# Kernel optimization log

Hardware: AMD Instinct MI355X
Metric: run time of the kernel (lower is better)

## Reference

```python
import jax, jax.numpy as jnp
import numpy as np

QUERY_DIM = 1024
KEY_DIM = 768
NUM_HEADS = 16
HEAD_DIM = QUERY_DIM // NUM_HEADS
SCALE = HEAD_DIM ** -0.5


def setup_inputs() -> dict:
    key = jax.random.key(0)
    ks = jax.random.split(key, 11)
    B, Nq, Nk = 4, 4096, 1024
    s_q = QUERY_DIM ** -0.5
    s_k = KEY_DIM ** -0.5
    return {
        "query": jax.random.normal(ks[0], (B, Nq, QUERY_DIM), jnp.float32),
        "key": jax.random.normal(ks[1], (B, Nk, KEY_DIM), jnp.float32),
        "value": jax.random.normal(ks[2], (B, Nk, KEY_DIM), jnp.float32),
        "Wq": jax.random.normal(ks[3], (QUERY_DIM, QUERY_DIM), jnp.float32) * s_q,
        "bq": jnp.zeros((QUERY_DIM,), jnp.float32),
        "Wk": jax.random.normal(ks[4], (KEY_DIM, QUERY_DIM), jnp.float32) * s_k,
        "bk": jnp.zeros((QUERY_DIM,), jnp.float32),
        "Wv": jax.random.normal(ks[5], (KEY_DIM, QUERY_DIM), jnp.float32) * s_k,
        "bv": jnp.zeros((QUERY_DIM,), jnp.float32),
        "Wo": jax.random.normal(ks[6], (QUERY_DIM, QUERY_DIM), jnp.float32) * s_q,
        "bo": jnp.zeros((QUERY_DIM,), jnp.float32),
    }


def reference(query, key, value, Wq, bq, Wk, bk, Wv, bv, Wo, bo):
    B, Nq, _ = query.shape
    Nk = key.shape[1]
    # projections to (B, H, N, d)
    q = (query @ Wq + bq).reshape(B, Nq, NUM_HEADS, HEAD_DIM).transpose(0, 2, 1, 3)
    k = (key @ Wk + bk).reshape(B, Nk, NUM_HEADS, HEAD_DIM).transpose(0, 2, 1, 3)
    v = (value @ Wv + bv).reshape(B, Nk, NUM_HEADS, HEAD_DIM).transpose(0, 2, 1, 3)
    attn = jnp.einsum("bhqd,bhkd->bhqk", q, k) * SCALE
    attn = jax.nn.softmax(attn, axis=-1)
    out = jnp.einsum("bhqk,bhkd->bhqd", attn, v)
    out = out.transpose(0, 2, 1, 3).reshape(B, Nq, QUERY_DIM)
    return out @ Wo + bo
```

## Files before the change

### kernel.cpp

```cpp
#include <hip/hip_runtime.h>
#include <hip/hip_bf16.h>
#include <stdint.h>


typedef unsigned short u16;
typedef __attribute__((ext_vector_type(8))) short short8;
typedef __attribute__((ext_vector_type(4))) float f32x4;

#define B_SZ 4
#define NQ   4096
#define NK   1024
#define QDIM 1024
#define KDIM 768
#define NH   16
#define HD   64
#define QSCALE (0.125f * 1.44269504f)

__device__ __forceinline__ u16 f2bf(float f) {
  union { float f; uint32_t u; } v; v.f = f;
  uint32_t u = v.u;
  return (u16)((u + 0x7FFFu + ((u >> 16) & 1u)) >> 16);
}

__device__ __forceinline__ uint32_t pk2(float a, float b) {
  union { __hip_bfloat162 h; uint32_t u; } cv;
  cv.h = __float22bfloat162_rn(float2{a, b});
  return cv.u;
}

__device__ __forceinline__ float fexp2(float x) {
  return __builtin_amdgcn_exp2f(x);
}

__device__ __forceinline__ void async16(u16* lds, const u16* g) {
  __builtin_amdgcn_global_load_lds(
      (__attribute__((address_space(1))) void*)(g),
      (__attribute__((address_space(3))) void*)(lds), 16, 0, 0);
}

__global__ __launch_bounds__(256) void f32_to_bf16_k(const float* __restrict__ in,
                                                     u16* __restrict__ out, int n4) {
  int i = blockIdx.x * 256 + threadIdx.x;
  if (i < n4) {
    f32x4 v = ((const f32x4*)in)[i];
    uint2 o = {pk2(v.x, v.y), pk2(v.z, v.w)};
    ((uint2*)out)[i] = o;
  }
}

__global__ __launch_bounds__(256) void f32_to_bf16_2k(const float* __restrict__ a,
                                                      const float* __restrict__ b,
                                                      u16* __restrict__ oa,
                                                      u16* __restrict__ ob, int n4) {
  int i = blockIdx.x * 256 + threadIdx.x;
  const float* in = blockIdx.y ? b : a;
  u16* out = blockIdx.y ? ob : oa;
  if (i < n4) {
    f32x4 v = ((const f32x4*)in)[i];
    uint2 o = {pk2(v.x, v.y), pk2(v.z, v.w)};
    ((uint2*)out)[i] = o;
  }
}

__global__ __launch_bounds__(256) void transpose_bf16_k(const float* __restrict__ W,
                                                        u16* __restrict__ Wt,
                                                        int K, int N) {
  __shared__ float t[32][33];
  int tx = threadIdx.x & 31, ty = threadIdx.x >> 5;
  int nb = blockIdx.x * 32, kb = blockIdx.y * 32;
#pragma unroll
  for (int i = 0; i < 4; ++i)
    t[ty + i * 8][tx] = W[(size_t)(kb + ty + i * 8) * N + nb + tx];
  __syncthreads();
#pragma unroll
  for (int i = 0; i < 4; ++i)
    Wt[(size_t)(nb + ty + i * 8) * K + kb + tx] = f2bf(t[tx][ty + i * 8]);
}

__global__ __launch_bounds__(256) void gemm_bt(const u16* __restrict__ A,
                                               const u16* __restrict__ Bt,
                                               const float* __restrict__ bias,
                                               float* __restrict__ Cf,
                                               u16* __restrict__ Cb,
                                               int M, int N, int K, int out_bf16,
                                               float scale) {
  __shared__ __align__(16) u16 Al[128 * 64];
  __shared__ __align__(16) u16 Bl[128 * 64];
  const int tid = threadIdx.x;
  const int w = tid >> 6, lane = tid & 63;
  const int g = lane >> 4, l15 = lane & 15;
  const int sw = l15 & 7;
  const int mbase = blockIdx.x * 128, nbase = blockIdx.y * 128;
  const int wm = (w & 1) * 64, wn = (w >> 1) * 64;

  f32x4 zero4 = {0.f, 0.f, 0.f, 0.f};
  f32x4 acc[4][4];
#pragma unroll
  for (int i = 0; i < 4; ++i)
#pragma unroll
    for (int j = 0; j < 4; ++j) acc[i][j] = zero4;

  for (int kb = 0; kb < K; kb += 64) {
#pragma unroll
    for (int i = 0; i < 4; ++i) {
      int cbase = w * 256 + i * 64;
      int c = cbase + lane;
      int row = c >> 3;
      int kc8 = ((c & 7) ^ (row & 7)) * 8;
      async16(&Al[cbase * 8], A + (size_t)(mbase + row) * K + kb + kc8);
      async16(&Bl[cbase * 8], Bt + (size_t)(nbase + row) * K + kb + kc8);
    }
    __syncthreads();
#pragma unroll
    for (int ks = 0; ks < 2; ++ks) {
      short8 af[4], bf[4];
#pragma unroll
      for (int mt = 0; mt < 4; ++mt)
        af[mt] = *(const short8*)&Al[(wm + mt * 16 + l15) * 64 + ((ks * 4 + g) ^ sw) * 8];
#pragma unroll
      for (int nt = 0; nt < 4; ++nt)
        bf[nt] = *(const short8*)&Bl[(wn + nt * 16 + l15) * 64 + ((ks * 4 + g) ^ sw) * 8];
#pragma unroll
      for (int mt = 0; mt < 4; ++mt)
#pragma unroll
        for (int nt = 0; nt < 4; ++nt)
          acc[mt][nt] = __builtin_amdgcn_mfma_f32_16x16x32_bf16(af[mt], bf[nt],
                                                                acc[mt][nt], 0, 0, 0);
    }
    __syncthreads();
  }

#pragma unroll
  for (int nt = 0; nt < 4; ++nt) {
    int col = nbase + wn + nt * 16 + l15;
    float bv = bias[col];
#pragma unroll
    for (int mt = 0; mt < 4; ++mt)
#pragma unroll
      for (int r = 0; r < 4; ++r) {
        int row = mbase + wm + mt * 16 + g * 4 + r;
        float v = (acc[mt][nt][r] + bv) * scale;
        if (out_bf16) Cb[(size_t)row * N + col] = f2bf(v);
        else          Cf[(size_t)row * N + col] = v;
      }
  }
}

__global__ __launch_bounds__(256) void gemm_kv(const u16* __restrict__ kA,
                                               const u16* __restrict__ vA,
                                               const u16* __restrict__ Wk,
                                               const u16* __restrict__ Wv,
                                               const float* __restrict__ bk,
                                               const float* __restrict__ bv,
                                               u16* __restrict__ Kp,
                                               u16* __restrict__ VT,
                                               int M, int N, int K) {
  __shared__ __align__(16) u16 Al[128 * 64];
  __shared__ __align__(16) u16 Bl[128 * 64];
  const int ct = blockIdx.z;
  const u16* A  = ct ? vA : kA;
  const u16* Bt = ct ? Wv : Wk;
  const float* bias = ct ? bv : bk;
  const int tid = threadIdx.x;
  const int w = tid >> 6, lane = tid & 63;
  const int g = lane >> 4, l15 = lane & 15;
  const int sw = l15 & 7;
  const int mbase = blockIdx.x * 128, nbase = blockIdx.y * 128;
  const int wm = (w & 1) * 64, wn = (w >> 1) * 64;

  f32x4 zero4 = {0.f, 0.f, 0.f, 0.f};
  f32x4 acc[4][4];
#pragma unroll
  for (int i = 0; i < 4; ++i)
#pragma unroll
    for (int j = 0; j < 4; ++j) acc[i][j] = zero4;

  for (int kb = 0; kb < K; kb += 64) {
#pragma unroll
    for (int i = 0; i < 4; ++i) {
      int cbase = w * 256 + i * 64;
      int c = cbase + lane;
      int row = c >> 3;
      int kc8 = ((c & 7) ^ (row & 7)) * 8;
      async16(&Al[cbase * 8], A + (size_t)(mbase + row) * K + kb + kc8);
      async16(&Bl[cbase * 8], Bt + (size_t)(nbase + row) * K + kb + kc8);
    }
    __syncthreads();
#pragma unroll
    for (int ks = 0; ks < 2; ++ks) {
      short8 af[4], bf[4];
#pragma unroll
      for (int mt = 0; mt < 4; ++mt)
        af[mt] = *(const short8*)&Al[(wm + mt * 16 + l15) * 64 + ((ks * 4 + g) ^ sw) * 8];
#pragma unroll
      for (int nt = 0; nt < 4; ++nt)
        bf[nt] = *(const short8*)&Bl[(wn + nt * 16 + l15) * 64 + ((ks * 4 + g) ^ sw) * 8];
      if (ct) {
#pragma unroll
        for (int nt = 0; nt < 4; ++nt)
#pragma unroll
          for (int mt = 0; mt < 4; ++mt)
            acc[nt][mt] = __builtin_amdgcn_mfma_f32_16x16x32_bf16(bf[nt], af[mt],
                                                                  acc[nt][mt], 0, 0, 0);
      } else {
#pragma unroll
        for (int mt = 0; mt < 4; ++mt)
#pragma unroll
          for (int nt = 0; nt < 4; ++nt)
            acc[mt][nt] = __builtin_amdgcn_mfma_f32_16x16x32_bf16(af[mt], bf[nt],
                                                                  acc[mt][nt], 0, 0, 0);
      }
    }
    __syncthreads();
  }

  if (ct) {
#pragma unroll
    for (int mt = 0; mt < 4; ++mt) {
      int m = mbase + wm + mt * 16 + l15;
#pragma unroll
      for (int nt = 0; nt < 4; ++nt)
#pragma unroll
        for (int r = 0; r < 4; ++r) {
          int n = nbase + wn + nt * 16 + g * 4 + r;
          VT[(size_t)n * M + m] = f2bf(acc[nt][mt][r] + bias[n]);
        }
    }
  } else {
#pragma unroll
    for (int nt = 0; nt < 4; ++nt) {
      int col = nbase + wn + nt * 16 + l15;
      float bvv = bias[col];
#pragma unroll
      for (int mt = 0; mt < 4; ++mt)
#pragma unroll
        for (int r = 0; r < 4; ++r) {
          int row = mbase + wm + mt * 16 + g * 4 + r;
          Kp[(size_t)row * N + col] = f2bf(acc[mt][nt][r] + bvv);
        }
    }
  }
}

__global__ __launch_bounds__(256) void attn_kernel(const u16* __restrict__ Qp,
                                                   const u16* __restrict__ Kp,
                                                   const u16* __restrict__ VT,
                                                   u16* __restrict__ AO) {
  __shared__ __align__(16) u16 K_lds[2][64 * 64];
  __shared__ __align__(16) u16 Vt_lds[2][64 * 64];
  __shared__ __align__(16) u16 P_lds[4][32 * 64];

  const int tid = threadIdx.x;
  const int w = tid >> 6, lane = tid & 63;
  const int g = lane >> 4, l15 = lane & 15;
  const int sw = l15 & 7;
  const int bh = blockIdx.y, b = bh >> 4, h = bh & 15;
  const int qrow0 = blockIdx.x * 128 + w * 32;
  const int MT = B_SZ * NK;

  const int cbase0 = (w * 2 + 0) * 64;
  const int cbase1 = (w * 2 + 1) * 64;
  const int c0 = cbase0 + lane, c1 = cbase1 + lane;
  const int row0 = c0 >> 3, kc80 = ((c0 & 7) ^ (row0 & 7)) * 8;
  const int row1 = c1 >> 3, kc81 = ((c1 & 7) ^ (row1 & 7)) * 8;

  const u16* kp0 = Kp + (size_t)(b * NK + row0) * QDIM + h * HD + kc80;
  const u16* kp1 = Kp + (size_t)(b * NK + row1) * QDIM + h * HD + kc81;
  const u16* vp0 = VT + (size_t)(h * HD + row0) * MT + b * NK + kc80;
  const u16* vp1 = VT + (size_t)(h * HD + row1) * MT + b * NK + kc81;

  const int rb = l15 * 64;
  const int cs0 = (g ^ sw) * 8;
  const int cs1 = ((4 + g) ^ sw) * 8;
  const int pwb = rb + (((g >> 1) ^ (sw & 1)) * 8) + (g & 1) * 4;
  const int pms = sw & 6;

  short8 ones8;
#pragma unroll
  for (int j = 0; j < 8; ++j) ones8[j] = (short)0x3F80;

  short8 qf[2][2];
#pragma unroll
  for (int qt = 0; qt < 2; ++qt)
#pragma unroll
    for (int ks = 0; ks < 2; ++ks) {
      size_t row = (size_t)(b * NQ + qrow0 + qt * 16 + l15);
      qf[qt][ks] = *(const short8*)(Qp + row * QDIM + h * HD + ks * 32 + g * 8);
    }

  f32x4 zero4 = {0.f, 0.f, 0.f, 0.f};
  f32x4 o4[4][2];
  f32x4 lacc[2];
#pragma unroll
  for (int dt = 0; dt < 4; ++dt)
#pragma unroll
    for (int qt = 0; qt < 2; ++qt) o4[dt][qt] = zero4;
  lacc[0] = zero4; lacc[1] = zero4;

  async16(&K_lds[0][cbase0 * 8], kp0);
  async16(&K_lds[0][cbase1 * 8], kp1);
  async16(&Vt_lds[0][cbase0 * 8], vp0);
  async16(&Vt_lds[0][cbase1 * 8], vp1);
  kp0 += 64 * QDIM; kp1 += 64 * QDIM; vp0 += 64; vp1 += 64;
  __syncthreads();

  int cur = 0;
  for (int kc = 0; kc < NK / 64; ++kc) {
    if (kc + 1 < NK / 64) {
      int nb = cur ^ 1;
      async16(&K_lds[nb][cbase0 * 8], kp0);
      async16(&K_lds[nb][cbase1 * 8], kp1);
      async16(&Vt_lds[nb][cbase0 * 8], vp0);
      async16(&Vt_lds[nb][cbase1 * 8], vp1);
      kp0 += 64 * QDIM; kp1 += 64 * QDIM; vp0 += 64; vp1 += 64;
    }
    const u16* Kl = &K_lds[cur][0];
    const u16* Vl = &Vt_lds[cur][0];
    u16* Pl = &P_lds[w][0];

    f32x4 sc[4][2];
    {
      short8 kf[4];
#pragma unroll
      for (int mt = 0; mt < 4; ++mt)
        kf[mt] = *(const short8*)&Kl[mt * 1024 + rb + cs0];
      __builtin_amdgcn_s_setprio(1);
#pragma unroll
      for (int mt = 0; mt < 4; ++mt)
#pragma unroll
        for (int qt = 0; qt < 2; ++qt)
          sc[mt][qt] = __builtin_amdgcn_mfma_f32_16x16x32_bf16(kf[mt], qf[qt][0],
                                                               zero4, 0, 0, 0);
      __builtin_amdgcn_s_setprio(0);
#pragma unroll
      for (int mt = 0; mt < 4; ++mt)
        kf[mt] = *(const short8*)&Kl[mt * 1024 + rb + cs1];
      __builtin_amdgcn_s_setprio(1);
#pragma unroll
      for (int mt = 0; mt < 4; ++mt)
#pragma unroll
        for (int qt = 0; qt < 2; ++qt)
          sc[mt][qt] = __builtin_amdgcn_mfma_f32_16x16x32_bf16(kf[mt], qf[qt][1],
                                                               sc[mt][qt], 0, 0, 0);
      __builtin_amdgcn_s_setprio(0);
    }

#pragma unroll
    for (int qt = 0; qt < 2; ++qt) {
#pragma unroll
      for (int mt = 0; mt < 4; ++mt) {
        float p0 = fexp2(sc[mt][qt][0]);
        float p1 = fexp2(sc[mt][qt][1]);
        float p2 = fexp2(sc[mt][qt][2]);
        float p3 = fexp2(sc[mt][qt][3]);
        uint2 pk = {pk2(p0, p1), pk2(p2, p3)};
        *(uint2*)&Pl[qt * 1024 + pwb + ((mt * 2) ^ pms) * 8] = pk;
      }
    }

#pragma unroll
    for (int ks = 0; ks < 2; ++ks) {
      const int cs = ks ? cs1 : cs0;
      short8 vf[4], pb[2];
#pragma unroll
      for (int dt = 0; dt < 4; ++dt)
        vf[dt] = *(const short8*)&Vl[dt * 1024 + rb + cs];
#pragma unroll
      for (int qt = 0; qt < 2; ++qt)
        pb[qt] = *(const short8*)&Pl[qt * 1024 + rb + cs];
      __builtin_amdgcn_s_setprio(1);
#pragma unroll
      for (int qt = 0; qt < 2; ++qt)
        lacc[qt] = __builtin_amdgcn_mfma_f32_16x16x32_bf16(ones8, pb[qt],
                                                           lacc[qt], 0, 0, 0);
#pragma unroll
      for (int dt = 0; dt < 4; ++dt)
#pragma unroll
        for (int qt = 0; qt < 2; ++qt)
          o4[dt][qt] = __builtin_amdgcn_mfma_f32_16x16x32_bf16(vf[dt], pb[qt],
                                                               o4[dt][qt], 0, 0, 0);
      __builtin_amdgcn_s_setprio(0);
    }
    if (kc + 1 < NK / 64) __syncthreads();
    cur ^= 1;
  }

#pragma unroll
  for (int qt = 0; qt < 2; ++qt) {
    float inv = __builtin_amdgcn_rcpf(lacc[qt][0]);
    size_t row = (size_t)(b * NQ + qrow0 + qt * 16 + l15);
#pragma unroll
    for (int dt = 0; dt < 4; ++dt) {
      uint2 pk = {pk2(o4[dt][qt][0] * inv, o4[dt][qt][1] * inv),
                  pk2(o4[dt][qt][2] * inv, o4[dt][qt][3] * inv)};
      *(uint2*)(AO + row * QDIM + h * HD + dt * 16 + g * 4) = pk;
    }
  }
}

extern "C" void kernel_launch(void* const* d_in, const int* in_sizes, int n_in,
                              void* d_out, int out_size, void* d_ws, size_t ws_size,
                              hipStream_t stream) {
  const float* query = (const float*)d_in[0];
  const float* key   = (const float*)d_in[1];
  const float* value = (const float*)d_in[2];
  const float* Wq = (const float*)d_in[3];
  const float* bq = (const float*)d_in[4];
  const float* Wk = (const float*)d_in[5];
  const float* bk = (const float*)d_in[6];
  const float* Wv = (const float*)d_in[7];
  const float* bv = (const float*)d_in[8];
  const float* Wo = (const float*)d_in[9];
  const float* bo = (const float*)d_in[10];

  char* ws = (char*)d_ws;
  size_t off = 0;
  auto alloc = [&](size_t bytes) -> void* {
    void* p = ws + off;
    off += (bytes + 255) & ~(size_t)255;
    return p;
  };
  const size_t NQTOT = (size_t)B_SZ * NQ;
  const size_t NKTOT = (size_t)B_SZ * NK;
  u16* qbf = (u16*)alloc(NQTOT * QDIM * 2);
  u16* kbf = (u16*)alloc(NKTOT * KDIM * 2);
  u16* vbf = (u16*)alloc(NKTOT * KDIM * 2);
  u16* wqt = (u16*)alloc((size_t)QDIM * QDIM * 2);
  u16* wkt = (u16*)alloc((size_t)KDIM * QDIM * 2);
  u16* wvt = (u16*)alloc((size_t)KDIM * QDIM * 2);
  u16* wot = (u16*)alloc((size_t)QDIM * QDIM * 2);
  u16* Qp  = (u16*)alloc(NQTOT * QDIM * 2);
  u16* Kp  = (u16*)alloc(NKTOT * QDIM * 2);
  u16* VT  = (u16*)alloc((size_t)QDIM * NKTOT * 2);
  u16* AO  = qbf;

  {
    int n4 = (int)(NQTOT * QDIM / 4);
    f32_to_bf16_k<<<(n4 + 255) / 256, 256, 0, stream>>>(query, qbf, n4);
  }
  {
    int n4 = (int)(NKTOT * KDIM / 4);
    f32_to_bf16_2k<<<dim3((n4 + 255) / 256, 2), 256, 0, stream>>>(key, value, kbf,
                                                                  vbf, n4);
  }
  transpose_bf16_k<<<dim3(QDIM / 32, QDIM / 32), 256, 0, stream>>>(Wq, wqt, QDIM, QDIM);
  transpose_bf16_k<<<dim3(QDIM / 32, KDIM / 32), 256, 0, stream>>>(Wk, wkt, KDIM, QDIM);
  transpose_bf16_k<<<dim3(QDIM / 32, KDIM / 32), 256, 0, stream>>>(Wv, wvt, KDIM, QDIM);
  transpose_bf16_k<<<dim3(QDIM / 32, QDIM / 32), 256, 0, stream>>>(Wo, wot, QDIM, QDIM);

  gemm_bt<<<dim3(NQTOT / 128, QDIM / 128), 256, 0, stream>>>(
      qbf, wqt, bq, nullptr, Qp, (int)NQTOT, QDIM, QDIM, 1, QSCALE);
  gemm_kv<<<dim3(NKTOT / 128, QDIM / 128, 2), 256, 0, stream>>>(
      kbf, vbf, wkt, wvt, bk, bv, Kp, VT, (int)NKTOT, QDIM, KDIM);

  attn_kernel<<<dim3(NQ / 128, B_SZ * NH), 256, 0, stream>>>(Qp, Kp, VT, AO);

  gemm_bt<<<dim3(NQTOT / 128, QDIM / 128), 256, 0, stream>>>(
      AO, wot, bo, (float*)d_out, nullptr, (int)NQTOT, QDIM, QDIM, 0, 1.0f);

  (void)in_sizes; (void)n_in; (void)out_size; (void)ws_size;
}
```

Baseline: 428.1 us.

## Software-pipeline attention loop: overlap QK^T of next chunk with PV of previous

Restructures the attention main loop so each iteration computes the QK^T scores for chunk kc while running the PV MFMAs for chunk kc-1, whose P tile was written in the previous iteration. This adds a prologue and epilogue and a triple-buffered V tile in LDS. The exp/pack work no longer sits between the two MFMA phases, so matrix and vector work can interleave and stalls should drop. It also adds launch_bounds(256,2) to cap registers for two blocks per CU, at some risk of register spills given the larger live fragment set.

```diff
diff --git a/kernel.cpp b/kernel.cpp
--- a/kernel.cpp
+++ b/kernel.cpp
@@ -242,12 +242,12 @@
   }
 }
 
-__global__ __launch_bounds__(256) void attn_kernel(const u16* __restrict__ Qp,
-                                                   const u16* __restrict__ Kp,
-                                                   const u16* __restrict__ VT,
-                                                   u16* __restrict__ AO) {
+__global__ __launch_bounds__(256, 2) void attn_kernel(const u16* __restrict__ Qp,
+                                                      const u16* __restrict__ Kp,
+                                                      const u16* __restrict__ VT,
+                                                      u16* __restrict__ AO) {
   __shared__ __align__(16) u16 K_lds[2][64 * 64];
-  __shared__ __align__(16) u16 Vt_lds[2][64 * 64];
+  __shared__ __align__(16) u16 V_lds[3][64 * 64];
   __shared__ __align__(16) u16 P_lds[4][32 * 64];
 
   const int tid = threadIdx.x;
@@ -297,56 +297,46 @@
     for (int qt = 0; qt < 2; ++qt) o4[dt][qt] = zero4;
   lacc[0] = zero4; lacc[1] = zero4;
 
+  u16* Pl = &P_lds[w][0];
+
   async16(&K_lds[0][cbase0 * 8], kp0);
   async16(&K_lds[0][cbase1 * 8], kp1);
-  async16(&Vt_lds[0][cbase0 * 8], vp0);
-  async16(&Vt_lds[0][cbase1 * 8], vp1);
+  async16(&V_lds[0][cbase0 * 8], vp0);
+  async16(&V_lds[0][cbase1 * 8], vp1);
   kp0 += 64 * QDIM; kp1 += 64 * QDIM; vp0 += 64; vp1 += 64;
   __syncthreads();
 
-  int cur = 0;
-  for (int kc = 0; kc < NK / 64; ++kc) {
-    if (kc + 1 < NK / 64) {
-      int nb = cur ^ 1;
-      async16(&K_lds[nb][cbase0 * 8], kp0);
-      async16(&K_lds[nb][cbase1 * 8], kp1);
-      async16(&Vt_lds[nb][cbase0 * 8], vp0);
-      async16(&Vt_lds[nb][cbase1 * 8], vp1);
-      kp0 += 64 * QDIM; kp1 += 64 * QDIM; vp0 += 64; vp1 += 64;
-    }
-    const u16* Kl = &K_lds[cur][0];
-    const u16* Vl = &Vt_lds[cur][0];
-    u16* Pl = &P_lds[w][0];
-
+  async16(&K_lds[1][cbase0 * 8], kp0);
+  async16(&K_lds[1][cbase1 * 8], kp1);
+  async16(&V_lds[1][cbase0 * 8], vp0);
+  async16(&V_lds[1][cbase1 * 8], vp1);
+  kp0 += 64 * QDIM; kp1 += 64 * QDIM; vp0 += 64; vp1 += 64;
+
+  {
+    const u16* Kl = &K_lds[0][0];
     f32x4 sc[4][2];
-    {
-      short8 kf[4];
-#pragma unroll
-      for (int mt = 0; mt < 4; ++mt)
-        kf[mt] = *(const short8*)&Kl[mt * 1024 + rb + cs0];
-      __builtin_amdgcn_s_setprio(1);
-#pragma unroll
-      for (int mt = 0; mt < 4; ++mt)
-#pragma unroll
-        for (int qt = 0; qt < 2; ++qt)
-          sc[mt][qt] = __builtin_amdgcn_mfma_f32_16x16x32_bf16(kf[mt], qf[qt][0],
-                                                               zero4, 0, 0, 0);
-      __builtin_amdgcn_s_setprio(0);
-#pragma unroll
-      for (int mt = 0; mt < 4; ++mt)
-        kf[mt] = *(const short8*)&Kl[mt * 1024 + rb + cs1];
-      __builtin_amdgcn_s_setprio(1);
-#pragma unroll
-      for (int mt = 0; mt < 4; ++mt)
-#pragma unroll
-        for (int qt = 0; qt < 2; ++qt)
-          sc[mt][qt] = __builtin_amdgcn_mfma_f32_16x16x32_bf16(kf[mt], qf[qt][1],
-                                                               sc[mt][qt], 0, 0, 0);
-      __builtin_amdgcn_s_setprio(0);
-    }
-
-#pragma unroll
-    for (int qt = 0; qt < 2; ++qt) {
+    short8 kf0[4], kf1[4];
+#pragma unroll
+    for (int mt = 0; mt < 4; ++mt) {
+      kf0[mt] = *(const short8*)&Kl[mt * 1024 + rb + cs0];
+      kf1[mt] = *(const short8*)&Kl[mt * 1024 + rb + cs1];
+    }
+    __builtin_amdgcn_s_setprio(1);
+#pragma unroll
+    for (int mt = 0; mt < 4; ++mt)
+#pragma unroll
+      for (int qt = 0; qt < 2; ++qt)
+        sc[mt][qt] = __builtin_amdgcn_mfma_f32_16x16x32_bf16(kf0[mt], qf[qt][0],
+                                                             zero4, 0, 0, 0);
+#pragma unroll
+    for (int mt = 0; mt < 4; ++mt)
+#pragma unroll
+      for (int qt = 0; qt < 2; ++qt)
+        sc[mt][qt] = __builtin_amdgcn_mfma_f32_16x16x32_bf16(kf1[mt], qf[qt][1],
+                                                             sc[mt][qt], 0, 0, 0);
+    __builtin_amdgcn_s_setprio(0);
+#pragma unroll
+    for (int qt = 0; qt < 2; ++qt)
 #pragma unroll
       for (int mt = 0; mt < 4; ++mt) {
         float p0 = fexp2(sc[mt][qt][0]);
@@ -356,33 +346,117 @@
         uint2 pk = {pk2(p0, p1), pk2(p2, p3)};
         *(uint2*)&Pl[qt * 1024 + pwb + ((mt * 2) ^ pms) * 8] = pk;
       }
-    }
-
+  }
+  __syncthreads();
+
+  for (int kc = 1; kc < NK / 64; ++kc) {
+    const int pv = (kc - 1) % 3;
+    if (kc + 1 < NK / 64) {
+      const int nk = (kc + 1) & 1, nv = (kc + 1) % 3;
+      async16(&K_lds[nk][cbase0 * 8], kp0);
+      async16(&K_lds[nk][cbase1 * 8], kp1);
+      async16(&V_lds[nv][cbase0 * 8], vp0);
+      async16(&V_lds[nv][cbase1 * 8], vp1);
+      kp0 += 64 * QDIM; kp1 += 64 * QDIM; vp0 += 64; vp1 += 64;
+    }
+    const u16* Kl = &K_lds[kc & 1][0];
+    const u16* Vl = &V_lds[pv][0];
+
+    short8 pb[2][2], vf[2][4], kf[2][4];
+#pragma unroll
+    for (int qt = 0; qt < 2; ++qt) {
+      pb[0][qt] = *(const short8*)&Pl[qt * 1024 + rb + cs0];
+      pb[1][qt] = *(const short8*)&Pl[qt * 1024 + rb + cs1];
+    }
+#pragma unroll
+    for (int dt = 0; dt < 4; ++dt) {
+      vf[0][dt] = *(const short8*)&Vl[dt * 1024 + rb + cs0];
+      vf[1][dt] = *(const short8*)&Vl[dt * 1024 + rb + cs1];
+    }
+#pragma unroll
+    for (int mt = 0; mt < 4; ++mt) {
+      kf[0][mt] = *(const short8*)&Kl[mt * 1024 + rb + cs0];
+      kf[1][mt] = *(const short8*)&Kl[mt * 1024 + rb + cs1];
+    }
+
+    f32x4 sc[4][2];
+    __builtin_amdgcn_s_setprio(1);
+#pragma unroll
+    for (int mt = 0; mt < 4; ++mt)
+#pragma unroll
+      for (int qt = 0; qt < 2; ++qt)
+        sc[mt][qt] = __builtin_amdgcn_mfma_f32_16x16x32_bf16(kf[0][mt], qf[qt][0],
+                                                             zero4, 0, 0, 0);
+#pragma unroll
+    for (int qt = 0; qt < 2; ++qt)
+      lacc[qt] = __builtin_amdgcn_mfma_f32_16x16x32_bf16(ones8, pb[0][qt],
+                                                         lacc[qt], 0, 0, 0);
+#pragma unroll
+    for (int dt = 0; dt < 4; ++dt)
+#pragma unroll
+      for (int qt = 0; qt < 2; ++qt)
+        o4[dt][qt] = __builtin_amdgcn_mfma_f32_16x16x32_bf16(vf[0][dt], pb[0][qt],
+                                                             o4[dt][qt], 0, 0, 0);
+#pragma unroll
+    for (int mt = 0; mt < 4; ++mt)
+#pragma unroll
+      for (int qt = 0; qt < 2; ++qt)
+        sc[mt][qt] = __builtin_amdgcn_mfma_f32_16x16x32_bf16(kf[1][mt], qf[qt][1],
+                                                             sc[mt][qt], 0, 0, 0);
+#pragma unroll
+    for (int qt = 0; qt < 2; ++qt)
+      lacc[qt] = __builtin_amdgcn_mfma_f32_16x16x32_bf16(ones8, pb[1][qt],
+                                                         lacc[qt], 0, 0, 0);
+#pragma unroll
+    for (int dt = 0; dt < 4; ++dt)
+#pragma unroll
+      for (int qt = 0; qt < 2; ++qt)
+        o4[dt][qt] = __builtin_amdgcn_mfma_f32_16x16x32_bf16(vf[1][dt], pb[1][qt],
+                                                             o4[dt][qt], 0, 0, 0);
+    __builtin_amdgcn_s_setprio(0);
+
+#pragma unroll
+    for (int qt = 0; qt < 2; ++qt)
+#pragma unroll
+      for (int mt = 0; mt < 4; ++mt) {
+        float p0 = fexp2(sc[mt][qt][0]);
+        float p1 = fexp2(sc[mt][qt][1]);
+        float p2 = fexp2(sc[mt][qt][2]);
+        float p3 = fexp2(sc[mt][qt][3]);
+        uint2 pk = {pk2(p0, p1), pk2(p2, p3)};
+        *(uint2*)&Pl[qt * 1024 + pwb + ((mt * 2) ^ pms) * 8] = pk;
+      }
+    __syncthreads();
+  }
+
+  {
+    const u16* Vl = &V_lds[(NK / 64 - 1) % 3][0];
+    short8 pb[2][2], vf[2][4];
+#pragma unroll
+    for (int qt = 0; qt < 2; ++qt) {
+      pb[0][qt] = *(const short8*)&Pl[qt * 1024 + rb + cs0];
+      pb[1][qt] = *(const short8*)&Pl[qt * 1024 + rb + cs1];
+    }
+#pragma unroll
+    for (int dt = 0; dt < 4; ++dt) {
+      vf[0][dt] = *(const short8*)&Vl[dt * 1024 + rb + cs0];
+      vf[1][dt] = *(const short8*)&Vl[dt * 1024 + rb + cs1];
+    }
+    __builtin_amdgcn_s_setprio(1);
 #pragma unroll
     for (int ks = 0; ks < 2; ++ks) {
-      const int cs = ks ? cs1 : cs0;
-      short8 vf[4], pb[2];
+#pragma unroll
+      for (int qt = 0; qt < 2; ++qt)
+        lacc[qt] = __builtin_amdgcn_mfma_f32_16x16x32_bf16(ones8, pb[ks][qt],
+                                                           lacc[qt], 0, 0, 0);
 #pragma unroll
       for (int dt = 0; dt < 4; ++dt)
-        vf[dt] = *(const short8*)&Vl[dt * 1024 + rb + cs];
-#pragma unroll
-      for (int qt = 0; qt < 2; ++qt)
-        pb[qt] = *(const short8*)&Pl[qt * 1024 + rb + cs];
-      __builtin_amdgcn_s_setprio(1);
-#pragma unroll
-      for (int qt = 0; qt < 2; ++qt)
-        lacc[qt] = __builtin_amdgcn_mfma_f32_16x16x32_bf16(ones8, pb[qt],
-                                                           lacc[qt], 0, 0, 0);
-#pragma unroll
-      for (int dt = 0; dt < 4; ++dt)
 #pragma unroll
         for (int qt = 0; qt < 2; ++qt)
-          o4[dt][qt] = __builtin_amdgcn_mfma_f32_16x16x32_bf16(vf[dt], pb[qt],
+          o4[dt][qt] = __builtin_amdgcn_mfma_f32_16x16x32_bf16(vf[ks][dt], pb[ks][qt],
                                                                o4[dt][qt], 0, 0, 0);
-      __builtin_amdgcn_s_setprio(0);
-    }
-    if (kc + 1 < NK / 64) __syncthreads();
-    cur ^= 1;
+    }
+    __builtin_amdgcn_s_setprio(0);
   }
 
 #pragma unroll
```

Measured after the change: 423.1 us. About the same (-1.2%).
